# Kernel tuning notes

Hardware: AMD Instinct MI355X
Metric: run time of the kernel (lower is better)

## Reference

```python
import jax, jax.numpy as jnp
import numpy as np

D_MODEL = 1024
NHEAD = 16
HEAD_DIM = D_MODEL // NHEAD
EPS = 1e-5


def layernorm(x, g, b):
    mu = jnp.mean(x, axis=-1, keepdims=True)
    var = jnp.mean(jnp.square(x - mu), axis=-1, keepdims=True)
    return (x - mu) * jax.lax.rsqrt(var + EPS) * g + b


def setup_inputs() -> dict:
    key = jax.random.key(0)
    ks = jax.random.split(key, 10)
    B, S, D = 8, 2048, D_MODEL
    s = 1.0 / np.sqrt(D)
    return {
        "x": jax.random.normal(ks[0], (B, S, D), dtype=jnp.float32),
        "wq": jax.random.normal(ks[1], (D, D), dtype=jnp.float32) * s,
        "wk": jax.random.normal(ks[2], (D, D), dtype=jnp.float32) * s,
        "wv": jax.random.normal(ks[3], (D, D), dtype=jnp.float32) * s,
        "ln1_g": jnp.ones((D,), dtype=jnp.float32),
        "ln1_b": jnp.zeros((D,), dtype=jnp.float32),
        "ln2_g": jnp.ones((D,), dtype=jnp.float32),
        "ln2_b": jnp.zeros((D,), dtype=jnp.float32),
        "w1": jax.random.normal(ks[4], (D, D), dtype=jnp.float32) * s,
        "b1": jnp.zeros((D,), dtype=jnp.float32),
        "w2": jax.random.normal(ks[5], (D, D), dtype=jnp.float32) * s,
        "b2": jnp.zeros((D,), dtype=jnp.float32),
    }


def reference(x, wq, wk, wv, ln1_g, ln1_b, ln2_g, ln2_b, w1, b1, w2, b2):
    B, S, D = x.shape
    H, Dh = NHEAD, HEAD_DIM
    xn = layernorm(x, ln1_g, ln1_b)
    # nn.Linear: y = x @ W.T (no bias for q/k/v)
    q = (xn @ wq.T).reshape(B, S, H, Dh)
    k = (xn @ wk.T).reshape(B, S, H, Dh)
    v = (xn @ wv.T).reshape(B, S, H, Dh)
    scale = 1.0 / jnp.sqrt(jnp.float32(Dh))
    scores = jnp.einsum("bqhd,bkhd->bhqk", q, k) * scale  # [B,H,S,S]
    attn = jax.nn.softmax(scores, axis=-1)
    att = jnp.einsum("bhqk,bkhd->bqhd", attn, v).reshape(B, S, D)
    xt = layernorm(xn + att, ln2_g, ln2_b)
    ffn = jax.nn.relu(xt @ w1.T + b1) @ w2.T + b2
    return xt + ffn
```

## Files before the change

kernel.cpp:

```cpp
#include <hip/hip_runtime.h>
#include <hip/hip_bf16.h>

typedef __bf16 bf16x8 __attribute__((ext_vector_type(8)));
typedef float f32x4 __attribute__((ext_vector_type(4)));
typedef float f32x16 __attribute__((ext_vector_type(16)));

#define MFMA_B16(a, b, c) __builtin_amdgcn_mfma_f32_16x16x32_bf16((a), (b), (c), 0, 0, 0)
#define MFMA32_B16(a, b, c) __builtin_amdgcn_mfma_f32_32x32x16_bf16((a), (b), (c), 0, 0, 0)
#define GLD16(g, l)                                                              \
    __builtin_amdgcn_global_load_lds((__attribute__((address_space(1))) void*)(g), \
                                     (__attribute__((address_space(3))) void*)(l), \
                                     16, 0, 0)

__device__ __forceinline__ float bfu2f(unsigned short u) {
    return __uint_as_float(((unsigned)u) << 16);
}
__device__ __forceinline__ unsigned short f2bfu(float f) {
    unsigned u = __float_as_uint(f);
    u += 0x7fffu + ((u >> 16) & 1u);
    return (unsigned short)(u >> 16);
}
__device__ __forceinline__ float fexp2(float x) {
#if __has_builtin(__builtin_amdgcn_exp2f)
    return __builtin_amdgcn_exp2f(x);
#else
    return __expf(x * 0.69314718f);
#endif
}
__device__ __forceinline__ unsigned cvtpk_bf16(float lo_, float hi_) {
    unsigned r;
    asm("v_cvt_pk_bf16_f32 %0, %1, %2" : "=v"(r) : "v"(lo_), "v"(hi_));
    return r;
}
__device__ __forceinline__ void plswap(unsigned& a, unsigned& b) {
#if __has_builtin(__builtin_amdgcn_permlane32_swap)
    typedef int v2i __attribute__((ext_vector_type(2)));
    v2i r = __builtin_amdgcn_permlane32_swap((int)a, (int)b, false, false);
    a = (unsigned)r.x;
    b = (unsigned)r.y;
#else
    unsigned pa_ = (unsigned)__shfl_xor((int)a, 32);
    unsigned pb_ = (unsigned)__shfl_xor((int)b, 32);
    bool hi = (threadIdx.x & 63) >= 32;
    unsigned na = hi ? pb_ : a;
    unsigned nb = hi ? b : pa_;
    a = na;
    b = nb;
#endif
}

__global__ __launch_bounds__(256) void cvt5_f32_bf16(const float* __restrict__ s0,
                                                     const float* __restrict__ s1,
                                                     const float* __restrict__ s2,
                                                     const float* __restrict__ s3,
                                                     const float* __restrict__ s4,
                                                     unsigned short* __restrict__ dst) {
    int wsel = blockIdx.x >> 10;
    int i = (blockIdx.x & 1023) * 256 + threadIdx.x;
    const float* src = s0;
    if (wsel == 1) src = s1;
    else if (wsel == 2) src = s2;
    else if (wsel == 3) src = s3;
    else if (wsel == 4) src = s4;
    float4 v = ((const float4*)src)[i];
    ((ushort4*)dst)[wsel * 262144 + i] =
        make_ushort4(f2bfu(v.x), f2bfu(v.y), f2bfu(v.z), f2bfu(v.w));
}

__global__ __launch_bounds__(256) void ln1_kernel(const float* __restrict__ in1,
                                                  const float* __restrict__ gam,
                                                  const float* __restrict__ bet,
                                                  unsigned short* __restrict__ outb) {
    int row = blockIdx.x, tid = threadIdx.x;
    size_t base = (size_t)row * 1024 + tid * 4;
    float4 v = *(const float4*)(in1 + base);
    float s = v.x + v.y + v.z + v.w;
    float sq = v.x * v.x + v.y * v.y + v.z * v.z + v.w * v.w;
#pragma unroll
    for (int m = 1; m < 64; m <<= 1) {
        s += __shfl_xor(s, m);
        sq += __shfl_xor(sq, m);
    }
    __shared__ float red[8];
    int w = tid >> 6;
    if ((tid & 63) == 0) { red[w] = s; red[w + 4] = sq; }
    __syncthreads();
    s = red[0] + red[1] + red[2] + red[3];
    sq = red[4] + red[5] + red[6] + red[7];
    float mean = s * (1.0f / 1024.0f);
    float var = fmaxf(sq * (1.0f / 1024.0f) - mean * mean, 0.0f);
    float rstd = rsqrtf(var + 1e-5f);
    float4 g4 = *(const float4*)(gam + tid * 4);
    float4 b4 = *(const float4*)(bet + tid * 4);
    *(ushort4*)(outb + base) = make_ushort4(
        f2bfu((v.x - mean) * rstd * g4.x + b4.x), f2bfu((v.y - mean) * rstd * g4.y + b4.y),
        f2bfu((v.z - mean) * rstd * g4.z + b4.z), f2bfu((v.w - mean) * rstd * g4.w + b4.w));
}

__global__ __launch_bounds__(256) void ln2_kernel(const unsigned short* __restrict__ in1,
                                                  const unsigned short* __restrict__ in2,
                                                  const float* __restrict__ gam,
                                                  const float* __restrict__ bet,
                                                  unsigned short* __restrict__ outb) {
    int row = blockIdx.x, tid = threadIdx.x;
    size_t base = (size_t)row * 1024 + tid * 4;
    ushort4 a = *(const ushort4*)(in1 + base);
    ushort4 c = *(const ushort4*)(in2 + base);
    float4 v = make_float4(bfu2f(a.x) + bfu2f(c.x), bfu2f(a.y) + bfu2f(c.y),
                           bfu2f(a.z) + bfu2f(c.z), bfu2f(a.w) + bfu2f(c.w));
    float s = v.x + v.y + v.z + v.w;
    float sq = v.x * v.x + v.y * v.y + v.z * v.z + v.w * v.w;
#pragma unroll
    for (int m = 1; m < 64; m <<= 1) {
        s += __shfl_xor(s, m);
        sq += __shfl_xor(sq, m);
    }
    __shared__ float red[8];
    int w = tid >> 6;
    if ((tid & 63) == 0) { red[w] = s; red[w + 4] = sq; }
    __syncthreads();
    s = red[0] + red[1] + red[2] + red[3];
    sq = red[4] + red[5] + red[6] + red[7];
    float mean = s * (1.0f / 1024.0f);
    float var = fmaxf(sq * (1.0f / 1024.0f) - mean * mean, 0.0f);
    float rstd = rsqrtf(var + 1e-5f);
    float4 g4 = *(const float4*)(gam + tid * 4);
    float4 b4 = *(const float4*)(bet + tid * 4);
    *(ushort4*)(outb + base) = make_ushort4(
        f2bfu((v.x - mean) * rstd * g4.x + b4.x), f2bfu((v.y - mean) * rstd * g4.y + b4.y),
        f2bfu((v.z - mean) * rstd * g4.z + b4.z), f2bfu((v.w - mean) * rstd * g4.w + b4.w));
}

template <int MODE>
__global__ __launch_bounds__(512, 2) void gemm8(const unsigned short* __restrict__ A,
                                                const unsigned short* __restrict__ Bw,
                                                const float* __restrict__ bias,
                                                const unsigned short* __restrict__ resid,
                                                void* __restrict__ O0, void* __restrict__ O1,
                                                void* __restrict__ O2, int M, int N, int K) {
    __shared__ unsigned short As[4][8192];
    __shared__ unsigned short Bs[4][8192];
    int nt = N >> 8;
    int bid = blockIdx.x;
    int nwg = gridDim.x;
    int swz = (bid & 7) * (nwg >> 3) + (bid >> 3);
    int mt = swz / nt, ntl = swz % nt;
    int mbase = mt << 8, nbase = ntl << 8;
    int tid = threadIdx.x;
    int w = tid >> 6, l = tid & 63;
    int wm = w >> 2, wn = w & 3;
    int lr = l & 15, lg = l >> 4;
    int lx = lr & 7;
    int brow = (wn & 1) * 64;

    int srow = tid >> 3;
    int csrc = (tid & 7) ^ (srow & 7);
    const unsigned short* aRow = A + (size_t)(mbase + srow) * K + csrc * 8;
    const unsigned short* bRow = Bw + (size_t)(nbase + srow) * K + csrc * 8;

    const int NT = K >> 6;
    auto stA = [&](int buf, int h, int t) {
        if (t >= NT) return;
        const unsigned short* s0 = aRow + (size_t)(h * 128) * K + t * 64;
        GLD16(s0, &As[buf * 2 + h][w * 512]);
        GLD16(s0 + (size_t)64 * K, &As[buf * 2 + h][4096 + w * 512]);
    };
    auto stB = [&](int buf, int h, int t) {
        if (t >= NT) return;
        const unsigned short* s0 = bRow + (size_t)(h * 128) * K + t * 64;
        GLD16(s0, &Bs[buf * 2 + h][w * 512]);
        GLD16(s0 + (size_t)64 * K, &Bs[buf * 2 + h][4096 + w * 512]);
    };

    f32x4 acc[8][4] = {};
    bf16x8 afr[4][2], bq0[2][2], bq1[2][2];

    auto rdA = [&](int buf, int mq) {
        const unsigned short* base = &As[buf * 2 + wm][0];
#pragma unroll
        for (int mf = 0; mf < 4; mf++)
#pragma unroll
            for (int ks = 0; ks < 2; ks++)
                afr[mf][ks] = *(const bf16x8*)(base + (mq * 64 + mf * 16 + lr) * 64 +
                                               (((ks * 4 + lg) ^ lx) << 3));
    };
    auto rdB = [&](int buf, int nq, bf16x8 (&bf)[2][2]) {
        const unsigned short* base = &Bs[buf * 2 + (wn >> 1)][0];
#pragma unroll
        for (int nf = 0; nf < 2; nf++)
#pragma unroll
            for (int ks = 0; ks < 2; ks++)
                bf[nf][ks] = *(const bf16x8*)(base + (brow + nq * 32 + nf * 16 + lr) * 64 +
                                              (((ks * 4 + lg) ^ lx) << 3));
    };
    auto MM = [&](int mq, int nq, bf16x8 (&bf)[2][2]) {
        __builtin_amdgcn_s_setprio(1);
#pragma unroll
        for (int mf = 0; mf < 4; mf++)
#pragma unroll
            for (int nf = 0; nf < 2; nf++)
#pragma unroll
                for (int ks = 0; ks < 2; ks++)
                    acc[mq * 4 + mf][nq * 2 + nf] =
                        MFMA_B16(afr[mf][ks], bf[nf][ks], acc[mq * 4 + mf][nq * 2 + nf]);
        __builtin_amdgcn_s_setprio(0);
    };
#define BARX __builtin_amdgcn_s_barrier()
#define LGK0 do { asm volatile("s_waitcnt lgkmcnt(0)" ::: "memory"); \
                  __builtin_amdgcn_sched_barrier(0); } while (0)
#define VMC(n) asm volatile("s_waitcnt vmcnt(" #n ")" ::: "memory")

    stA(0, 0, 0); stA(0, 1, 0); stB(0, 0, 0); stB(0, 1, 0); stB(1, 0, 1); stB(1, 1, 1);
    VMC(4);
    BARX;

    int NIT = NT >> 1;
    for (int i = 0; i < NIT; i++) {
        int t0 = 2 * i, t1 = t0 + 1;
        bool lastI = (i == NIT - 1);
        rdA(0, 0); rdB(0, 0, bq0); stA(1, 0, t1);
        BARX; LGK0; MM(0, 0, bq0); BARX;
        rdB(0, 1, bq1); stA(1, 1, t1);
        BARX; LGK0; MM(0, 1, bq1); BARX;
        rdA(0, 1); stB(0, 0, t0 + 2);
        BARX; LGK0; MM(1, 1, bq1); BARX;
        stB(0, 1, t0 + 2);
        if (lastI) { VMC(0); } else { VMC(4); }
        BARX; MM(1, 0, bq0); BARX;
        rdA(1, 0); rdB(1, 0, bq0); stA(0, 0, t0 + 2);
        BARX; LGK0; MM(0, 0, bq0); BARX;
        rdB(1, 1, bq1); stA(0, 1, t0 + 2);
        BARX; LGK0; MM(0, 1, bq1); BARX;
        rdA(1, 1); stB(1, 0, t1 + 2);
        BARX; LGK0; MM(1, 1, bq1); BARX;
        stB(1, 1, t1 + 2);
        if (!lastI) { VMC(4); }
        BARX; MM(1, 0, bq0); BARX;
    }

#pragma unroll
    for (int m = 0; m < 8; m++) {
        int row = mbase + wm * 128 + (m >> 2) * 64 + (m & 3) * 16 + lg * 4;
#pragma unroll
        for (int n = 0; n < 4; n++) {
            int col = nbase + wn * 64 + (n >> 1) * 32 + (n & 1) * 16 + lr;
            if constexpr (MODE == 0) {
                int wsel = col >> 10;
                int cl = col & 1023;
                if (wsel == 2) {
                    int hh = cl >> 6, dd = cl & 63;
                    int bb = row >> 11, ss = row & 2047;
                    unsigned short t4[4];
#pragma unroll
                    for (int j = 0; j < 4; j++) t4[j] = f2bfu(acc[m][n][j]);
                    size_t vtidx = ((size_t)((bb * 16 + hh) * 64 + dd)) * 2048 + ss;
                    *(uint2*)((unsigned short*)O2 + vtidx) = *(uint2*)t4;
                } else {
                    unsigned short* out = (wsel == 0) ? (unsigned short*)O0 : (unsigned short*)O1;
                    float sc = (wsel == 0) ? 0.18033688f : 1.0f;
#pragma unroll
                    for (int j = 0; j < 4; j++)
                        out[(size_t)(row + j) * 1024 + cl] = f2bfu(acc[m][n][j] * sc);
                }
            } else {
                float bv = bias[col];
#pragma unroll
                for (int j = 0; j < 4; j++) {
                    float v = acc[m][n][j] + bv;
                    size_t idx = (size_t)(row + j) * N + col;
                    if constexpr (MODE == 1) {
                        ((unsigned short*)O0)[idx] = f2bfu(fmaxf(v, 0.0f));
                    } else {
                        ((float*)O0)[idx] = v + bfu2f(resid[idx]);
                    }
                }
            }
        }
    }
#undef BARX
#undef LGK0
#undef VMC
}

__global__ __launch_bounds__(512) void attn_kernel(const unsigned short* __restrict__ qq,
                                                   const unsigned short* __restrict__ kk,
                                                   const unsigned short* __restrict__ vT,
                                                   unsigned short* __restrict__ attb) {
    __shared__ unsigned short Ks[4][64 * 64];
    __shared__ unsigned short Vs[4][64 * 64];

    int bid = blockIdx.x;
    int swz = (bid & 7) * (gridDim.x >> 3) + (bid >> 3);
    int qi = swz & 7, h = (swz >> 3) & 15, b = swz >> 7;
    int tid = threadIdx.x, w = tid >> 6, l = tid & 63;
    int lo = l & 31, hi = l >> 5;
    int q0 = qi * 256 + w * 32;

    const unsigned short* qp = qq + ((size_t)((b * 2048 + q0 + lo) * 16 + h)) * 64 + hi * 8;
    bf16x8 qf[4];
#pragma unroll
    for (int kc = 0; kc < 4; kc++) qf[kc] = *(const bf16x8*)(qp + kc * 16);

    int srow = w * 8 + (l >> 3);
    int schunk = (l & 7) ^ ((l >> 3) & 7);
    const unsigned short* ksrc0 = kk + ((size_t)((b * 2048 + srow) * 16 + h)) * 64 + schunk * 8;
    const unsigned short* vsrc0 = vT + ((size_t)((b * 16 + h) * 64 + srow)) * 2048 + schunk * 8;

    auto stageT = [&](int s) {
        if (s > 31) return;
        GLD16(ksrc0 + (size_t)s * 65536, &Ks[s & 3][w * 512]);
        GLD16(vsrc0 + (size_t)s * 64, &Vs[s & 3][w * 512]);
    };

    f32x16 od0 = {}, od1 = {};
    float ssum = 0.f;

    stageT(0); stageT(1);

    for (int s = 0; s < 32; s++) {
        stageT(s + 2);
        if (s < 30) asm volatile("s_waitcnt vmcnt(4)" ::: "memory");
        else if (s == 30) asm volatile("s_waitcnt vmcnt(2)" ::: "memory");
        else asm volatile("s_waitcnt vmcnt(0)" ::: "memory");
        __builtin_amdgcn_s_barrier();
        __builtin_amdgcn_sched_barrier(0);

        const unsigned short* Kb = &Ks[s & 3][0];
        const unsigned short* Vb = &Vs[s & 3][0];

        f32x16 sacc[2];
        __builtin_amdgcn_s_setprio(1);
#pragma unroll
        for (int tt = 0; tt < 2; tt++) {
            f32x16 sv = {};
            int row = tt * 32 + lo;
#pragma unroll
            for (int kc = 0; kc < 4; kc++) {
                bf16x8 a = *(const bf16x8*)(Kb + row * 64 + (((kc * 2 + hi) ^ (row & 7)) << 3));
                sv = MFMA32_B16(a, qf[kc], sv);
            }
            sacc[tt] = sv;
        }
        __builtin_amdgcn_s_setprio(0);
        float p[32];
        float ps0 = 0.f, ps1 = 0.f;
#pragma unroll
        for (int r = 0; r < 16; r++) {
            float e0 = fexp2(sacc[0][r]);
            float e1 = fexp2(sacc[1][r]);
            p[r] = e0;
            p[16 + r] = e1;
            ps0 += e0;
            ps1 += e1;
        }
        float psum = ps0 + ps1;
        psum += __shfl_xor(psum, 32);
        ssum += psum;
#pragma unroll
        for (int tt = 0; tt < 2; tt++) {
            unsigned wv[8];
#pragma unroll
            for (int i = 0; i < 8; i++) wv[i] = cvtpk_bf16(p[tt * 16 + 2 * i], p[tt * 16 + 2 * i + 1]);
            plswap(wv[0], wv[2]);
            plswap(wv[1], wv[3]);
            plswap(wv[4], wv[6]);
            plswap(wv[5], wv[7]);
            union { unsigned u[4]; bf16x8 v; } c0, c1;
            c0.u[0] = wv[0]; c0.u[1] = wv[1]; c0.u[2] = wv[2]; c0.u[3] = wv[3];
            c1.u[0] = wv[4]; c1.u[1] = wv[5]; c1.u[2] = wv[6]; c1.u[3] = wv[7];
            __builtin_amdgcn_s_setprio(1);
#pragma unroll
            for (int sub = 0; sub < 2; sub++) {
                int ks = tt * 2 + sub;
                bf16x8 pa = sub ? c1.v : c0.v;
                int slot = ((ks * 2 + hi) ^ (lo & 7)) << 3;
                bf16x8 v0 = *(const bf16x8*)(Vb + lo * 64 + slot);
                bf16x8 v1 = *(const bf16x8*)(Vb + (32 + lo) * 64 + slot);
                od0 = MFMA32_B16(pa, v0, od0);
                od1 = MFMA32_B16(pa, v1, od1);
            }
            __builtin_amdgcn_s_setprio(0);
        }
    }

#pragma unroll
    for (int r = 0; r < 16; r++) {
        int crow = (r & 3) + ((r >> 2) << 3) + (hi << 2);
        float rs = 1.0f / __shfl(ssum, crow);
        int q = q0 + crow;
        size_t base = ((size_t)((b * 2048 + q) * 16 + h)) * 64;
        attb[base + lo] = f2bfu(od0[r] * rs);
        attb[base + 32 + lo] = f2bfu(od1[r] * rs);
    }
}

extern "C" void kernel_launch(void* const* d_in, const int* in_sizes, int n_in,
                              void* d_out, int out_size, void* d_ws, size_t ws_size,
                              hipStream_t stream) {
    const float* x = (const float*)d_in[0];
    const float* wq = (const float*)d_in[1];
    const float* wk = (const float*)d_in[2];
    const float* wv = (const float*)d_in[3];
    const float* ln1_g = (const float*)d_in[4];
    const float* ln1_b = (const float*)d_in[5];
    const float* ln2_g = (const float*)d_in[6];
    const float* ln2_b = (const float*)d_in[7];
    const float* w1 = (const float*)d_in[8];
    const float* b1 = (const float*)d_in[9];
    const float* w2 = (const float*)d_in[10];
    const float* b2 = (const float*)d_in[11];

    const size_t NB = 33554432;
    char* ws = (char*)d_ws;
    unsigned short* xn_b = (unsigned short*)(ws);
    unsigned short* q_b = (unsigned short*)(ws + NB);
    unsigned short* k_b = (unsigned short*)(ws + 2 * NB);
    unsigned short* vT_b = (unsigned short*)(ws + 3 * NB);
    unsigned short* att_b = (unsigned short*)(ws + 4 * NB);
    unsigned short* wq_b = (unsigned short*)(ws + 5 * NB);
    unsigned short* w1_b = wq_b + 3145728;
    unsigned short* w2_b = w1_b + 1048576;
    unsigned short* xt_b = q_b;
    unsigned short* h_b = k_b;

    dim3 blk(256);
    cvt5_f32_bf16<<<5120, blk, 0, stream>>>(wq, wk, wv, w1, w2, wq_b);
    ln1_kernel<<<16384, blk, 0, stream>>>(x, ln1_g, ln1_b, xn_b);

    gemm8<0><<<768, dim3(512), 0, stream>>>(xn_b, wq_b, nullptr, nullptr,
                                            q_b, k_b, vT_b, 16384, 3072, 1024);

    attn_kernel<<<1024, dim3(512), 0, stream>>>(q_b, k_b, vT_b, att_b);

    ln2_kernel<<<16384, blk, 0, stream>>>(xn_b, att_b, ln2_g, ln2_b, xt_b);

    gemm8<1><<<256, dim3(512), 0, stream>>>(xt_b, w1_b, b1, nullptr,
                                            h_b, nullptr, nullptr, 16384, 1024, 1024);
    gemm8<2><<<256, dim3(512), 0, stream>>>(h_b, w2_b, b2, xt_b,
                                            d_out, nullptr, nullptr, 16384, 1024, 1024);
}
```

Before: 376.8 us.

## Software-pipeline QK and softmax-PV halves across tiles with deeper prefetch

Splits each K/V tile's work into two QK halves and two softmax+PV halves, then interleaves them so the next tile's first QK MFMA batch is issued while the current tile's exp and PV work proceeds. Prefetch depth grows from two to three tiles in the four-slot LDS ring. The row-sum cross-lane shuffle moves out of the loop and runs once at the end. This aims to overlap transcendental and VALU work with MFMA and hide more memory latency, at the cost of more live registers and a tighter buffer-reuse margin that relies on the single barrier per iteration.

Result: slower. 407.0 us (+8.0%).

```diff
diff --git a/kernel.cpp b/kernel.cpp
--- a/kernel.cpp
+++ b/kernel.cpp
@@ -315,74 +315,73 @@
     f32x16 od0 = {}, od1 = {};
     float ssum = 0.f;
 
-    stageT(0); stageT(1);
-
+    auto halfQK = [&](int t, int tt) -> f32x16 {
+        const unsigned short* Kb = &Ks[t & 3][0];
+        f32x16 sv = {};
+        int row = tt * 32 + lo;
+        __builtin_amdgcn_s_setprio(1);
+#pragma unroll
+        for (int kc = 0; kc < 4; kc++) {
+            bf16x8 a = *(const bf16x8*)(Kb + row * 64 + (((kc * 2 + hi) ^ (row & 7)) << 3));
+            sv = MFMA32_B16(a, qf[kc], sv);
+        }
+        __builtin_amdgcn_s_setprio(0);
+        return sv;
+    };
+    auto SMPV = [&](const f32x16& sc, int t, int tt) {
+        const unsigned short* Vb = &Vs[t & 3][0];
+        float p[16];
+        float ps = 0.f;
+#pragma unroll
+        for (int r = 0; r < 16; r++) {
+            float e = fexp2(sc[r]);
+            p[r] = e;
+            ps += e;
+        }
+        ssum += ps;
+        unsigned wv[8];
+#pragma unroll
+        for (int i = 0; i < 8; i++) wv[i] = cvtpk_bf16(p[2 * i], p[2 * i + 1]);
+        plswap(wv[0], wv[2]);
+        plswap(wv[1], wv[3]);
+        plswap(wv[4], wv[6]);
+        plswap(wv[5], wv[7]);
+        union { unsigned u[4]; bf16x8 v; } c0, c1;
+        c0.u[0] = wv[0]; c0.u[1] = wv[1]; c0.u[2] = wv[2]; c0.u[3] = wv[3];
+        c1.u[0] = wv[4]; c1.u[1] = wv[5]; c1.u[2] = wv[6]; c1.u[3] = wv[7];
+        __builtin_amdgcn_s_setprio(1);
+#pragma unroll
+        for (int sub = 0; sub < 2; sub++) {
+            int ks = tt * 2 + sub;
+            bf16x8 pa = sub ? c1.v : c0.v;
+            int slot = ((ks * 2 + hi) ^ (lo & 7)) << 3;
+            bf16x8 v0 = *(const bf16x8*)(Vb + lo * 64 + slot);
+            bf16x8 v1 = *(const bf16x8*)(Vb + (32 + lo) * 64 + slot);
+            od0 = MFMA32_B16(pa, v0, od0);
+            od1 = MFMA32_B16(pa, v1, od1);
+        }
+        __builtin_amdgcn_s_setprio(0);
+    };
+
+    stageT(0); stageT(1); stageT(2);
+    asm volatile("s_waitcnt vmcnt(4)" ::: "memory");
+    __builtin_amdgcn_s_barrier();
+    __builtin_amdgcn_sched_barrier(0);
+
+    f32x16 sA = halfQK(0, 0);
     for (int s = 0; s < 32; s++) {
-        stageT(s + 2);
-        if (s < 30) asm volatile("s_waitcnt vmcnt(4)" ::: "memory");
-        else if (s == 30) asm volatile("s_waitcnt vmcnt(2)" ::: "memory");
+        if (s < 30) asm volatile("s_waitcnt vmcnt(2)" ::: "memory");
         else asm volatile("s_waitcnt vmcnt(0)" ::: "memory");
         __builtin_amdgcn_s_barrier();
         __builtin_amdgcn_sched_barrier(0);
-
-        const unsigned short* Kb = &Ks[s & 3][0];
-        const unsigned short* Vb = &Vs[s & 3][0];
-
-        f32x16 sacc[2];
-        __builtin_amdgcn_s_setprio(1);
-#pragma unroll
-        for (int tt = 0; tt < 2; tt++) {
-            f32x16 sv = {};
-            int row = tt * 32 + lo;
-#pragma unroll
-            for (int kc = 0; kc < 4; kc++) {
-                bf16x8 a = *(const bf16x8*)(Kb + row * 64 + (((kc * 2 + hi) ^ (row & 7)) << 3));
-                sv = MFMA32_B16(a, qf[kc], sv);
-            }
-            sacc[tt] = sv;
-        }
-        __builtin_amdgcn_s_setprio(0);
-        float p[32];
-        float ps0 = 0.f, ps1 = 0.f;
-#pragma unroll
-        for (int r = 0; r < 16; r++) {
-            float e0 = fexp2(sacc[0][r]);
-            float e1 = fexp2(sacc[1][r]);
-            p[r] = e0;
-            p[16 + r] = e1;
-            ps0 += e0;
-            ps1 += e1;
-        }
-        float psum = ps0 + ps1;
-        psum += __shfl_xor(psum, 32);
-        ssum += psum;
-#pragma unroll
-        for (int tt = 0; tt < 2; tt++) {
-            unsigned wv[8];
-#pragma unroll
-            for (int i = 0; i < 8; i++) wv[i] = cvtpk_bf16(p[tt * 16 + 2 * i], p[tt * 16 + 2 * i + 1]);
-            plswap(wv[0], wv[2]);
-            plswap(wv[1], wv[3]);
-            plswap(wv[4], wv[6]);
-            plswap(wv[5], wv[7]);
-            union { unsigned u[4]; bf16x8 v; } c0, c1;
-            c0.u[0] = wv[0]; c0.u[1] = wv[1]; c0.u[2] = wv[2]; c0.u[3] = wv[3];
-            c1.u[0] = wv[4]; c1.u[1] = wv[5]; c1.u[2] = wv[6]; c1.u[3] = wv[7];
-            __builtin_amdgcn_s_setprio(1);
-#pragma unroll
-            for (int sub = 0; sub < 2; sub++) {
-                int ks = tt * 2 + sub;
-                bf16x8 pa = sub ? c1.v : c0.v;
-                int slot = ((ks * 2 + hi) ^ (lo & 7)) << 3;
-                bf16x8 v0 = *(const bf16x8*)(Vb + lo * 64 + slot);
-                bf16x8 v1 = *(const bf16x8*)(Vb + (32 + lo) * 64 + slot);
-                od0 = MFMA32_B16(pa, v0, od0);
-                od1 = MFMA32_B16(pa, v1, od1);
-            }
-            __builtin_amdgcn_s_setprio(0);
-        }
-    }
-
+        stageT(s + 3);
+        f32x16 sB = halfQK(s, 1);
+        SMPV(sA, s, 0);
+        if (s < 31) sA = halfQK(s + 1, 0);
+        SMPV(sB, s, 1);
+    }
+
+    ssum += __shfl_xor(ssum, 32);
 #pragma unroll
     for (int r = 0; r < 16; r++) {
         int crow = (r & 3) + ((r >> 2) << 3) + (hi << 2);
```
